# Performance work log

Hardware: AMD Instinct MI355X
Metric: run time of the kernel (lower is better)

Reference implementation:

```python
import jax, jax.numpy as jnp
import numpy as np


def _kernel_features(data, proj, is_query):
    # data: [B,S,H,D], proj: [R,D] -> features [B,S,H,R]  (FAVOR+ positive softmax kernel)
    d = data.shape[-1]
    r = proj.shape[0]
    data_normalizer = 1.0 / jnp.sqrt(jnp.sqrt(jnp.float32(d)))
    ratio = 1.0 / jnp.sqrt(jnp.float32(r))
    data_hat = jnp.einsum('bshd,rd->bshr', data_normalizer * data, proj)
    diag = (jnp.sum(data * data, axis=-1) * 0.5) * (data_normalizer * data_normalizer)
    diag = diag[..., None]  # [B,S,H,1]
    if is_query:
        m = jnp.max(data_hat, axis=-1, keepdims=True)
    else:
        m = jnp.max(data_hat)
    return ratio * (jnp.exp(data_hat - diag - m) + 1e-4)


def reference(query, key, value, Wq, bq, Wk, bk, Wv, bv, Wo, bo, proj):
    proj = jax.lax.stop_gradient(proj)
    # QKV projections: [B,S,Dm] -> [B,S,H,Dh]
    q = jnp.einsum('bsd,dhk->bshk', query, Wq) + bq
    k = jnp.einsum('bsd,dhk->bshk', key, Wk) + bk
    v = jnp.einsum('bsd,dhv->bshv', value, Wv) + bv
    q_hat = _kernel_features(q, proj, True)   # [B,S,H,R]
    k_hat = _kernel_features(k, proj, False)  # [B,S,H,R]
    # kv aggregation: 'aecr,aecd->acrd'
    kv = jnp.einsum('bshr,bshv->bhrv', k_hat, v)          # [B,H,R,Dv]
    out = jnp.einsum('bshr,bhrv->bshv', q_hat, kv)        # [B,S,H,Dv]
    # normalization: k1 = sum_s k_hat ('abcd,abc->acd'), denom = q_hat . k1
    k1 = jnp.sum(k_hat, axis=1)                           # [B,H,R]
    denom = jnp.einsum('bshr,bhr->bsh', q_hat, k1)        # [B,S,H]
    out = out / denom[..., None]
    # output projection: combine heads
    return jnp.einsum('bshv,hvd->bsd', out, Wo) + bo


def setup_inputs() -> dict:
    key0 = jax.random.key(0)
    ks = jax.random.split(key0, 10)
    B, S, Dm, H, Dh, R = 4, 4096, 1024, 16, 64, 256
    scale = 1.0 / np.sqrt(Dm)
    # Gaussian orthogonal random matrix [R, Dh], scaling=0 (chi row norms)
    blk = jax.random.normal(ks[8], (R, Dh))
    qmat, _ = jnp.linalg.qr(blk)  # R >= Dh -> q is [R, Dh]
    mult = jnp.linalg.norm(jax.random.normal(ks[9], (R, Dh)), axis=1)
    proj = mult[:, None] * qmat
    return {
        'query': jax.random.normal(ks[0], (B, S, Dm)),
        'key': jax.random.normal(ks[1], (B, S, Dm)),
        'value': jax.random.normal(ks[2], (B, S, Dm)),
        'Wq': jax.random.normal(ks[3], (Dm, H, Dh)) * scale,
        'bq': jnp.zeros((H, Dh)),
        'Wk': jax.random.normal(ks[4], (Dm, H, Dh)) * scale,
        'bk': jnp.zeros((H, Dh)),
        'Wv': jax.random.normal(ks[5], (Dm, H, Dh)) * scale,
        'bv': jnp.zeros((H, Dh)),
        'Wo': jax.random.normal(ks[6], (H, Dh, Dm)) * scale,
        'bo': jnp.zeros((Dm,)),
        'proj': proj,
    }
```

## Files before the change

kernel.cpp:

```cpp
#include <hip/hip_runtime.h>

typedef unsigned short u16;
typedef unsigned int u32;
typedef __attribute__((ext_vector_type(4))) float f32x4;
typedef __attribute__((ext_vector_type(8))) short bf16x8;

#define B_ 4
#define S_ 4096
#define H_ 16
#define DH_ 64
#define R_ 256
#define DM_ 1024
#define M_ 16384
#define ROWSTR 1024

__device__ __forceinline__ float bf2f(u16 u) {
  union { u32 i; float f; } v; v.i = ((u32)u) << 16; return v.f;
}
__device__ __forceinline__ u16 f2bf(float f) {
  union { float f; u32 i; } v; v.f = f;
  u32 x = v.i;
  return (u16)((x + 0x7FFFu + ((x >> 16) & 1u)) >> 16);
}
__device__ __forceinline__ void lds_load16(const void* g, void* l) {
  __builtin_amdgcn_global_load_lds((__attribute__((address_space(1))) void*)(g),
                                   (__attribute__((address_space(3))) void*)(l), 16, 0, 0);
}
__device__ __forceinline__ int vt_idx(int dv, int s) {
  return dv * 64 + (s ^ (dv & 0x38));
}

__global__ __launch_bounds__(256) void dtype_probe_k(const u16* __restrict__ q,
                                                     int* __restrict__ flag) {
  __shared__ int cnt_s;
  int tid = threadIdx.x;
  if (tid == 0) cnt_s = 0;
  __syncthreads();
  int c = 0;
  for (int i = tid; i < 1024; i += 256) {
    u32 e = ((u32)q[i] >> 7) & 0xFF;
    c += (e >= 134) ? 1 : 0;
  }
  atomicAdd(&cnt_s, c);
  __syncthreads();
  if (tid == 0) flag[0] = (cnt_s > 32) ? 1 : 0;
}

template <int WLO>
__global__ __launch_bounds__(256) void split_k(const void* __restrict__ src,
                                               u16* __restrict__ hi, u16* __restrict__ lo,
                                               const int* __restrict__ flag) {
  const bool f32m = flag[0] != 0;
  size_t i = ((size_t)blockIdx.x * 256 + threadIdx.x) * 8;
  if (f32m) {
    f32x4 a = *(const f32x4*)((const float*)src + i);
    f32x4 b = *(const f32x4*)((const float*)src + i + 4);
    bf16x8 h, l;
    for (int e = 0; e < 4; ++e) {
      u16 ha = f2bf(a[e]); h[e] = (short)ha; l[e] = (short)f2bf(a[e] - bf2f(ha));
      u16 hb = f2bf(b[e]); h[4 + e] = (short)hb; l[4 + e] = (short)f2bf(b[e] - bf2f(hb));
    }
    *(bf16x8*)(hi + i) = h;
    if (WLO) *(bf16x8*)(lo + i) = l;
  } else {
    bf16x8 h = *(const bf16x8*)((const u16*)src + i);
    *(bf16x8*)(hi + i) = h;
    if (WLO) {
      bf16x8 z = {0, 0, 0, 0, 0, 0, 0, 0};
      *(bf16x8*)(lo + i) = z;
    }
  }
}

__global__ __launch_bounds__(256) void transpose4_k(
    const void* __restrict__ s0, const void* __restrict__ s1,
    const void* __restrict__ s2, const void* __restrict__ s3,
    u16* __restrict__ dh0, u16* __restrict__ dl0, u16* __restrict__ dh1, u16* __restrict__ dl1,
    u16* __restrict__ dh2, u16* __restrict__ dl2, u16* __restrict__ dh3, u16* __restrict__ dl3,
    const int* __restrict__ flag) {
  __shared__ float tile[32][33];
  const bool f32m = flag[0] != 0;
  int z = blockIdx.z;
  const void* src = (z == 0) ? s0 : (z == 1) ? s1 : (z == 2) ? s2 : s3;
  u16* dh = (z == 0) ? dh0 : (z == 1) ? dh1 : (z == 2) ? dh2 : dh3;
  u16* dl = (z == 0) ? dl0 : (z == 1) ? dl1 : (z == 2) ? dl2 : dl3;
  int tx = threadIdx.x, ty = threadIdx.y;
  int x0 = blockIdx.x * 32, y0 = blockIdx.y * 32;
  for (int i = ty; i < 32; i += 8) {
    size_t idx = (size_t)(y0 + i) * DM_ + x0 + tx;
    tile[i][tx] = f32m ? ((const float*)src)[idx] : bf2f(((const u16*)src)[idx]);
  }
  __syncthreads();
  for (int i = ty; i < 32; i += 8) {
    float t = tile[tx][i];
    u16 hi = f2bf(t);
    size_t o = (size_t)(x0 + i) * DM_ + y0 + tx;
    dh[o] = hi;
    dl[o] = f2bf(t - bf2f(hi));
  }
}

__global__ __launch_bounds__(256) void projcvt_k(const void* __restrict__ p,
                                                 u16* __restrict__ ph, u16* __restrict__ pl,
                                                 const int* __restrict__ flag) {
  const bool f32m = flag[0] != 0;
  int i = blockIdx.x * 256 + threadIdx.x;
  if (i < R_ * DH_) {
    float t = f32m ? ((const float*)p)[i] : bf2f(((const u16*)p)[i]);
    u16 hi = f2bf(t);
    ph[i] = hi;
    pl[i] = f2bf(t - bf2f(hi));
  }
}

template <int PREC, int OUTMODE>
__global__ __launch_bounds__(256) void gemm_k(
    const u16* __restrict__ Ah, const u16* __restrict__ Al,
    const u16* __restrict__ Bth, const u16* __restrict__ Btl,
    const void* __restrict__ bias, void* __restrict__ C, u16* __restrict__ Clo,
    const int* __restrict__ flag) {
  __shared__ __attribute__((aligned(16))) u16 Ash[128 * 32];
  __shared__ __attribute__((aligned(16))) u16 Bsh[128 * 32];
  __shared__ __attribute__((aligned(16))) u16 Asl[128 * 32];
  __shared__ __attribute__((aligned(16))) u16 Bsl[128 * 32];
  const bool f32m = flag[0] != 0;
  const int K = DM_, N = DM_;
  const int tid = threadIdx.x, wave = tid >> 6, lane = tid & 63;
  const int lr = lane & 15, qd = lane >> 4;
  const int bm = blockIdx.x, bn = blockIdx.y;
  const int m0 = (wave & 1) * 64, n0 = (wave >> 1) * 64;
  const u16* Abh = Ah + (size_t)bm * 128 * K;
  const u16* Bbh = Bth + (size_t)bn * 128 * K;
  const u16* Abl = (PREC == 3) ? Al + (size_t)bm * 128 * K : nullptr;
  const u16* Bbl = (PREC == 3) ? Btl + (size_t)bn * 128 * K : nullptr;
  f32x4 zero = {0.f, 0.f, 0.f, 0.f};
  f32x4 acc[4][4];
  for (int i = 0; i < 4; ++i) for (int j = 0; j < 4; ++j) acc[i][j] = zero;
  for (int k0 = 0; k0 < K; k0 += 32) {
    __syncthreads();
    for (int t = 0; t < 2; ++t) {
      int c = wave + t * 4;
      int row = c * 16 + (lane >> 2);
      int kc = (lane & 3) * 8;
      size_t go = (size_t)row * K + k0 + kc;
      lds_load16(Abh + go, (void*)&Ash[c * 512]);
      lds_load16(Bbh + go, (void*)&Bsh[c * 512]);
      if (PREC == 3) {
        lds_load16(Abl + go, (void*)&Asl[c * 512]);
        lds_load16(Bbl + go, (void*)&Bsl[c * 512]);
      }
    }
    __syncthreads();
    bf16x8 ah[4], bh[4];
    for (int i = 0; i < 4; ++i) ah[i] = *(const bf16x8*)&Ash[(m0 + i * 16 + lr) * 32 + qd * 8];
    for (int j = 0; j < 4; ++j) bh[j] = *(const bf16x8*)&Bsh[(n0 + j * 16 + lr) * 32 + qd * 8];
    for (int i = 0; i < 4; ++i)
      for (int j = 0; j < 4; ++j)
        acc[i][j] = __builtin_amdgcn_mfma_f32_16x16x32_bf16(ah[i], bh[j], acc[i][j], 0, 0, 0);
    if (PREC == 3) {
      bf16x8 al[4], bl[4];
      for (int i = 0; i < 4; ++i) al[i] = *(const bf16x8*)&Asl[(m0 + i * 16 + lr) * 32 + qd * 8];
      for (int j = 0; j < 4; ++j) bl[j] = *(const bf16x8*)&Bsl[(n0 + j * 16 + lr) * 32 + qd * 8];
      for (int i = 0; i < 4; ++i)
        for (int j = 0; j < 4; ++j) {
          acc[i][j] = __builtin_amdgcn_mfma_f32_16x16x32_bf16(ah[i], bl[j], acc[i][j], 0, 0, 0);
          acc[i][j] = __builtin_amdgcn_mfma_f32_16x16x32_bf16(al[i], bh[j], acc[i][j], 0, 0, 0);
        }
    }
  }
  for (int j = 0; j < 4; ++j) {
    int n = bn * 128 + n0 + j * 16 + lr;
    float bv = f32m ? ((const float*)bias)[n] : bf2f(((const u16*)bias)[n]);
    for (int i = 0; i < 4; ++i) {
      int mr = bm * 128 + m0 + i * 16 + qd * 4;
      for (int r2 = 0; r2 < 4; ++r2) {
        float x = acc[i][j][r2] + bv;
        size_t o = (size_t)(mr + r2) * N + n;
        if (OUTMODE == 0) {
          ((u16*)C)[o] = f2bf(x);
        } else if (OUTMODE == 1) {
          u16 hi = f2bf(x);
          ((u16*)C)[o] = hi;
          Clo[o] = f2bf(x - bf2f(hi));
        } else {
          if (f32m) ((float*)C)[o] = x;
          else ((u16*)C)[o] = f2bf(x);
        }
      }
    }
  }
}

__global__ __launch_bounds__(256) void feat_max_k(
    const u16* __restrict__ khi, const u16* __restrict__ klo,
    const u16* __restrict__ ph, const u16* __restrict__ pl, float* __restrict__ pm) {
  __shared__ __attribute__((aligned(16))) u16 kth[64 * 64];
  __shared__ __attribute__((aligned(16))) u16 ktl[64 * 64];
  __shared__ float red[4];
  const int tid = threadIdx.x, wave = tid >> 6, lane = tid & 63;
  const int lr = lane & 15, qd = lane >> 4;
  int bid = blockIdx.x;
  int chunk = bid & 63, bh = bid >> 6;
  int b = bh >> 4, h = bh & 15;
  size_t base = (((size_t)b * S_ + (size_t)chunk * 64) * H_ + h) * DH_;
  for (int t = 0; t < 2; ++t) {
    int cc = wave + t * 4;
    int rr = cc * 8 + (lane >> 3);
    int csw = (((lane & 7) ^ (rr & 7)) << 3);
    size_t go = base + (size_t)rr * ROWSTR + csw;
    lds_load16(khi + go, (void*)&kth[cc * 512]);
    lds_load16(klo + go, (void*)&ktl[cc * 512]);
  }
  __syncthreads();
  const int r0 = wave * 64;
  f32x4 zero = {0.f, 0.f, 0.f, 0.f};
  f32x4 acc[4][4];
  for (int i = 0; i < 4; ++i) for (int j = 0; j < 4; ++j) acc[i][j] = zero;
  __builtin_amdgcn_s_setprio(1);
  for (int ks = 0; ks < 2; ++ks) {
    bf16x8 ah[4], al[4], bh_[4], bl_[4];
    for (int i = 0; i < 4; ++i) {
      int cof = (ks * 32 + qd * 8) ^ ((lr & 7) << 3);
      ah[i] = *(const bf16x8*)&kth[(i * 16 + lr) * 64 + cof];
      al[i] = *(const bf16x8*)&ktl[(i * 16 + lr) * 64 + cof];
    }
    for (int j = 0; j < 4; ++j) {
      size_t o = (size_t)(r0 + j * 16 + lr) * DH_ + ks * 32 + qd * 8;
      bh_[j] = *(const bf16x8*)(ph + o);
      bl_[j] = *(const bf16x8*)(pl + o);
    }
    for (int i = 0; i < 4; ++i)
      for (int j = 0; j < 4; ++j) {
        acc[i][j] = __builtin_amdgcn_mfma_f32_16x16x32_bf16(ah[i], bh_[j], acc[i][j], 0, 0, 0);
        acc[i][j] = __builtin_amdgcn_mfma_f32_16x16x32_bf16(al[i], bh_[j], acc[i][j], 0, 0, 0);
        acc[i][j] = __builtin_amdgcn_mfma_f32_16x16x32_bf16(ah[i], bl_[j], acc[i][j], 0, 0, 0);
      }
  }
  __builtin_amdgcn_s_setprio(0);
  float mx = -3.0e38f;
  for (int i = 0; i < 4; ++i) for (int j = 0; j < 4; ++j) for (int r2 = 0; r2 < 4; ++r2)
    mx = fmaxf(mx, acc[i][j][r2]);
  for (int m2 = 1; m2 < 64; m2 <<= 1) mx = fmaxf(mx, __shfl_xor(mx, m2, 64));
  if (lane == 0) red[wave] = mx;
  __syncthreads();
  if (tid == 0)
    pm[bid] = 0.3535533905932738f * fmaxf(fmaxf(red[0], red[1]), fmaxf(red[2], red[3]));
}

__global__ __launch_bounds__(256) void reduce_max_k(const float* __restrict__ pm,
                                                    float* __restrict__ mout) {
  __shared__ float buf[256];
  int t = threadIdx.x;
  float m = -3.0e38f;
  for (int i = t; i < 4096; i += 256) m = fmaxf(m, pm[i]);
  buf[t] = m;
  __syncthreads();
  if (t < 64) {
    float v = fmaxf(fmaxf(buf[t], buf[t + 64]), fmaxf(buf[t + 128], buf[t + 192]));
    for (int m2 = 1; m2 < 64; m2 <<= 1) v = fmaxf(v, __shfl_xor(v, m2, 64));
    if (t == 0) mout[0] = v;
  }
}

__global__ __launch_bounds__(256) void kv_accum_k(
    const u16* __restrict__ khi, const u16* __restrict__ klo,
    const u16* __restrict__ vv,
    const u16* __restrict__ ph, const u16* __restrict__ pl,
    const float* __restrict__ mptr,
    float* __restrict__ pkv, float* __restrict__ pk1, int ipb) {
  __shared__ __attribute__((aligned(16))) u16 pool[256 * 72];
  __shared__ __attribute__((aligned(16))) u16 vTh[64 * 64];
  __shared__ float dpart[4][64];
  __shared__ float diagl[64];
  u16* kth = pool;
  u16* ktl = pool + 4096;
  u16* khatT = pool;
  const int tid = threadIdx.x, wave = tid >> 6, lane = tid & 63;
  const int lr = lane & 15, qd = lane >> 4;
  int bid = blockIdx.x;
  int bh = bid & 63, c = bid >> 6;
  int b = bh >> 4, h = bh & 15;
  const float mglob = mptr[0];
  const float nrm = 0.3535533905932738f;
  const float ratio = 0.0625f;
  size_t base0 = (((size_t)b * S_ + (size_t)c * ipb * 64) * H_ + h) * DH_;
  f32x4 zero = {0.f, 0.f, 0.f, 0.f};
  f32x4 acc[4][4];
  for (int i = 0; i < 4; ++i) for (int j = 0; j < 4; ++j) acc[i][j] = zero;
  float k1p[4][4];
  for (int i = 0; i < 4; ++i) for (int r2 = 0; r2 < 4; ++r2) k1p[i][r2] = 0.f;
  const int r0 = wave * 64;
  bf16x8 pfa_h[2][4], pfa_l[2][4];
  for (int ks = 0; ks < 2; ++ks)
    for (int i = 0; i < 4; ++i) {
      size_t o = (size_t)(r0 + i * 16 + lr) * DH_ + ks * 32 + qd * 8;
      pfa_h[ks][i] = *(const bf16x8*)(ph + o);
      pfa_l[ks][i] = *(const bf16x8*)(pl + o);
    }
  for (int it = 0; it < ipb; ++it) {
    size_t ibase = base0 + (size_t)it * 64 * ROWSTR;
    __syncthreads();
    for (int t = 0; t < 2; ++t) {
      int cc = wave + t * 4;
      int rr = cc * 8 + (lane >> 3);
      int csw = (((lane & 7) ^ (rr & 7)) << 3);
      size_t go = ibase + (size_t)rr * ROWSTR + csw;
      lds_load16(khi + go, (void*)&kth[cc * 512]);
      lds_load16(klo + go, (void*)&ktl[cc * 512]);
    }
    {
      int s = tid >> 2;
      int dv0 = (tid & 3) * 16;
      size_t go = ibase + (size_t)s * ROWSTR + dv0;
      bf16x8 h0 = *(const bf16x8*)(vv + go);
      bf16x8 h1 = *(const bf16x8*)(vv + go + 8);
      for (int e = 0; e < 8; ++e) {
        vTh[vt_idx(dv0 + e, s)] = (u16)h0[e];
        vTh[vt_idx(dv0 + 8 + e, s)] = (u16)h1[e];
      }
    }
    __syncthreads();
    {
      int s = tid & 63, qr = tid >> 6;
      int swz = (s & 7) << 3;
      bf16x8 h0 = *(const bf16x8*)&kth[s * 64 + ((qr * 16) ^ swz)];
      bf16x8 h1 = *(const bf16x8*)&kth[s * 64 + ((qr * 16 + 8) ^ swz)];
      bf16x8 l0 = *(const bf16x8*)&ktl[s * 64 + ((qr * 16) ^ swz)];
      bf16x8 l1 = *(const bf16x8*)&ktl[s * 64 + ((qr * 16 + 8) ^ swz)];
      float sum = 0.f;
      for (int e = 0; e < 8; ++e) { float f = bf2f((u16)h0[e]) + bf2f((u16)l0[e]); sum += f * f; }
      for (int e = 0; e < 8; ++e) { float f = bf2f((u16)h1[e]) + bf2f((u16)l1[e]); sum += f * f; }
      dpart[qr][s] = sum;
    }
    __syncthreads();
    if (tid < 64)
      diagl[tid] = 0.0625f * (dpart[0][tid] + dpart[1][tid] + dpart[2][tid] + dpart[3][tid]);
    f32x4 a1[4][4];
    for (int i = 0; i < 4; ++i) for (int j = 0; j < 4; ++j) a1[i][j] = zero;
    __builtin_amdgcn_s_setprio(1);
    for (int ks = 0; ks < 2; ++ks) {
      bf16x8 bh_[4], bl_[4];
      for (int j = 0; j < 4; ++j) {
        int cof = (ks * 32 + qd * 8) ^ ((lr & 7) << 3);
        bh_[j] = *(const bf16x8*)&kth[(j * 16 + lr) * 64 + cof];
        bl_[j] = *(const bf16x8*)&ktl[(j * 16 + lr) * 64 + cof];
      }
      for (int i = 0; i < 4; ++i)
        for (int j = 0; j < 4; ++j) {
          a1[i][j] = __builtin_amdgcn_mfma_f32_16x16x32_bf16(pfa_h[ks][i], bh_[j], a1[i][j], 0, 0, 0);
          a1[i][j] = __builtin_amdgcn_mfma_f32_16x16x32_bf16(pfa_l[ks][i], bh_[j], a1[i][j], 0, 0, 0);
          a1[i][j] = __builtin_amdgcn_mfma_f32_16x16x32_bf16(pfa_h[ks][i], bl_[j], a1[i][j], 0, 0, 0);
        }
    }
    __builtin_amdgcn_s_setprio(0);
    __syncthreads();
    for (int i = 0; i < 4; ++i)
      for (int r2 = 0; r2 < 4; ++r2) {
        int r = r0 + i * 16 + qd * 4 + r2;
        for (int j = 0; j < 4; ++j) {
          int s = j * 16 + lr;
          float arg = fminf(nrm * a1[i][j][r2] - diagl[s] - mglob, 30.f);
          float kh = ratio * (__expf(arg) + 1e-4f);
          u16 khb = f2bf(kh);
          khatT[r * 72 + s] = khb;
          k1p[i][r2] += bf2f(khb);
        }
      }
    __syncthreads();
    __builtin_amdgcn_s_setprio(1);
    for (int ks = 0; ks < 2; ++ks) {
      bf16x8 af[4], bh_[4];
      for (int i = 0; i < 4; ++i)
        af[i] = *(const bf16x8*)&khatT[(r0 + i * 16 + lr) * 72 + ks * 32 + qd * 8];
      for (int j = 0; j < 4; ++j) {
        int dv = j * 16 + lr;
        bh_[j] = *(const bf16x8*)&vTh[vt_idx(dv, ks * 32 + qd * 8)];
      }
      for (int i = 0; i < 4; ++i)
        for (int j = 0; j < 4; ++j)
          acc[i][j] = __builtin_amdgcn_mfma_f32_16x16x32_bf16(af[i], bh_[j], acc[i][j], 0, 0, 0);
    }
    __builtin_amdgcn_s_setprio(0);
  }
  size_t obase = ((size_t)c * 64 + bh) * R_;
  for (int i = 0; i < 4; ++i)
    for (int j = 0; j < 4; ++j)
      for (int r2 = 0; r2 < 4; ++r2) {
        int r = r0 + i * 16 + qd * 4 + r2;
        int dv = j * 16 + lr;
        pkv[(obase + r) * DH_ + dv] = acc[i][j][r2];
      }
  for (int i = 0; i < 4; ++i)
    for (int r2 = 0; r2 < 4; ++r2) {
      float v = k1p[i][r2];
      v += __shfl_xor(v, 1, 64); v += __shfl_xor(v, 2, 64);
      v += __shfl_xor(v, 4, 64); v += __shfl_xor(v, 8, 64);
      if (lr == 0) pk1[obase + r0 + i * 16 + qd * 4 + r2] = v;
    }
}

__global__ __launch_bounds__(256) void kv_reduce_k(
    const float* __restrict__ pkv, const float* __restrict__ pk1,
    u16* __restrict__ kvTh, u16* __restrict__ kvTl, float* __restrict__ k1, int nchunk) {
  __shared__ float tile[64][65];
  int bh = blockIdx.x, tl = blockIdx.y, t = threadIdx.x;
  if (tl == 0) {
    float s = 0.f;
    for (int c = 0; c < nchunk; ++c) s += pk1[((size_t)c * 64 + bh) * R_ + t];
    k1[(size_t)bh * R_ + t] = s;
  }
  for (int e = 0; e < 16; ++e) {
    int idx = e * 256 + t;
    int rl = idx >> 6, dv = idx & 63;
    float s = 0.f;
    for (int c = 0; c < nchunk; ++c)
      s += pkv[(((size_t)c * 64 + bh) * R_ + tl * 64 + rl) * DH_ + dv];
    tile[rl][dv] = s;
  }
  __syncthreads();
  for (int e = 0; e < 16; ++e) {
    int idx = e * 256 + t;
    int dv = idx >> 6, rl = idx & 63;
    float s = tile[rl][dv];
    u16 hi = f2bf(s);
    size_t o = ((size_t)bh * DH_ + dv) * R_ + tl * 64 + rl;
    kvTh[o] = hi;
    kvTl[o] = f2bf(s - bf2f(hi));
  }
}

__global__ __launch_bounds__(256, 4) void q_out_k(
    const u16* __restrict__ qhi, const u16* __restrict__ qlo,
    const u16* __restrict__ ph, const u16* __restrict__ pl,
    const u16* __restrict__ kvTh, const u16* __restrict__ kvTl,
    const float* __restrict__ k1, u16* __restrict__ op) {
  __shared__ __attribute__((aligned(16))) u16 pool[64 * 264];
  __shared__ float wrm[4][64];
  __shared__ float dpart[4][64];
  __shared__ float diagl[64];
  __shared__ float dinv[64];
  u16* qth = pool;
  u16* qtl = pool + 4096;
  u16* qh = pool;
  const int tid = threadIdx.x, wave = tid >> 6, lane = tid & 63;
  const int lr = lane & 15, qd = lane >> 4;
  int bid = blockIdx.x;
  int chunk = bid & 63, bh = bid >> 6;
  int b = bh >> 4, h = bh & 15;
  const float nrm = 0.3535533905932738f;
  const float ratio = 0.0625f;
  size_t base = (((size_t)b * S_ + (size_t)chunk * 64) * H_ + h) * DH_;
  const u16* kvThb = kvTh + (size_t)bh * DH_ * R_;
  const u16* kvTlb = kvTl + (size_t)bh * DH_ * R_;
  const float* k1b = k1 + (size_t)bh * R_;
  for (int t = 0; t < 2; ++t) {
    int cc = wave + t * 4;
    int rr = cc * 8 + (lane >> 3);
    int csw = (((lane & 7) ^ (rr & 7)) << 3);
    size_t go = base + (size_t)rr * ROWSTR + csw;
    lds_load16(qhi + go, (void*)&qth[cc * 512]);
    lds_load16(qlo + go, (void*)&qtl[cc * 512]);
  }
  __syncthreads();
  {
    int s = tid & 63, qr = tid >> 6;
    int swz = (s & 7) << 3;
    bf16x8 h0 = *(const bf16x8*)&qth[s * 64 + ((qr * 16) ^ swz)];
    bf16x8 h1 = *(const bf16x8*)&qth[s * 64 + ((qr * 16 + 8) ^ swz)];
    bf16x8 l0 = *(const bf16x8*)&qtl[s * 64 + ((qr * 16) ^ swz)];
    bf16x8 l1 = *(const bf16x8*)&qtl[s * 64 + ((qr * 16 + 8) ^ swz)];
    float sum = 0.f;
    for (int e = 0; e < 8; ++e) { float f = bf2f((u16)h0[e]) + bf2f((u16)l0[e]); sum += f * f; }
    for (int e = 0; e < 8; ++e) { float f = bf2f((u16)h1[e]) + bf2f((u16)l1[e]); sum += f * f; }
    dpart[qr][s] = sum;
  }
  __syncthreads();
  if (tid < 64)
    diagl[tid] = 0.0625f * (dpart[0][tid] + dpart[1][tid] + dpart[2][tid] + dpart[3][tid]);
  f32x4 zero = {0.f, 0.f, 0.f, 0.f};
  f32x4 a1[4][4];
  for (int i = 0; i < 4; ++i) for (int j = 0; j < 4; ++j) a1[i][j] = zero;
  const int r0 = wave * 64;
  __builtin_amdgcn_s_setprio(1);
  for (int ks = 0; ks < 2; ++ks) {
    bf16x8 ah[4], al[4], bh_[4], bl_[4];
    for (int i = 0; i < 4; ++i) {
      int cof = (ks * 32 + qd * 8) ^ ((lr & 7) << 3);
      ah[i] = *(const bf16x8*)&qth[(i * 16 + lr) * 64 + cof];
      al[i] = *(const bf16x8*)&qtl[(i * 16 + lr) * 64 + cof];
    }
    for (int j = 0; j < 4; ++j) {
      size_t o = (size_t)(r0 + j * 16 + lr) * DH_ + ks * 32 + qd * 8;
      bh_[j] = *(const bf16x8*)(ph + o);
      bl_[j] = *(const bf16x8*)(pl + o);
    }
    for (int i = 0; i < 4; ++i)
      for (int j = 0; j < 4; ++j) {
        a1[i][j] = __builtin_amdgcn_mfma_f32_16x16x32_bf16(ah[i], bh_[j], a1[i][j], 0, 0, 0);
        a1[i][j] = __builtin_amdgcn_mfma_f32_16x16x32_bf16(al[i], bh_[j], a1[i][j], 0, 0, 0);
        a1[i][j] = __builtin_amdgcn_mfma_f32_16x16x32_bf16(ah[i], bl_[j], a1[i][j], 0, 0, 0);
      }
  }
  __builtin_amdgcn_s_setprio(0);
  for (int i = 0; i < 4; ++i)
    for (int r2 = 0; r2 < 4; ++r2) {
      float v = fmaxf(fmaxf(a1[i][0][r2], a1[i][1][r2]), fmaxf(a1[i][2][r2], a1[i][3][r2]));
      v = fmaxf(v, __shfl_xor(v, 1, 64)); v = fmaxf(v, __shfl_xor(v, 2, 64));
      v = fmaxf(v, __shfl_xor(v, 4, 64)); v = fmaxf(v, __shfl_xor(v, 8, 64));
      if (lr == 0) wrm[wave][i * 16 + qd * 4 + r2] = v;
    }
  __syncthreads();
  float k1v[4];
  for (int j = 0; j < 4; ++j) k1v[j] = k1b[r0 + j * 16 + lr];
  for (int i = 0; i < 4; ++i)
    for (int r2 = 0; r2 < 4; ++r2) {
      int s = i * 16 + qd * 4 + r2;
      float rmax = fmaxf(fmaxf(wrm[0][s], wrm[1][s]), fmaxf(wrm[2][s], wrm[3][s]));
      float dg = diagl[s];
      float dsum = 0.f;
      for (int j = 0; j < 4; ++j) {
        float arg = fminf(nrm * (a1[i][j][r2] - rmax) - dg, 30.f);
        float qv = ratio * (__expf(arg) + 1e-4f);
        u16 qvb = f2bf(qv);
        qh[s * 264 + r0 + j * 16 + lr] = qvb;
        dsum += bf2f(qvb) * k1v[j];
      }
      dsum += __shfl_xor(dsum, 1, 64);
      dsum += __shfl_xor(dsum, 2, 64);
      dsum += __shfl_xor(dsum, 4, 64);
      dsum += __shfl_xor(dsum, 8, 64);
      if (lr == 0) dpart[wave][s] = dsum;
    }
  __syncthreads();
  if (tid < 64) {
    float dn = dpart[0][tid] + dpart[1][tid] + dpart[2][tid] + dpart[3][tid];
    dinv[tid] = 1.0f / fmaxf(dn, 1e-35f);
  }
  __syncthreads();
  f32x4 a2[2][2];
  for (int i = 0; i < 2; ++i) for (int j = 0; j < 2; ++j) a2[i][j] = zero;
  const int sw2 = (wave & 1) * 32, dw = (wave >> 1) * 32;
  __builtin_amdgcn_s_setprio(1);
  for (int ks = 0; ks < 8; ++ks) {
    bf16x8 af[2], bh_[2], bl_[2];
    for (int i = 0; i < 2; ++i)
      af[i] = *(const bf16x8*)&qh[(sw2 + i * 16 + lr) * 264 + ks * 32 + qd * 8];
    for (int j = 0; j < 2; ++j) {
      size_t o = (size_t)(dw + j * 16 + lr) * R_ + ks * 32 + qd * 8;
      bh_[j] = *(const bf16x8*)(kvThb + o);
      bl_[j] = *(const bf16x8*)(kvTlb + o);
    }
    for (int i = 0; i < 2; ++i)
      for (int j = 0; j < 2; ++j) {
        a2[i][j] = __builtin_amdgcn_mfma_f32_16x16x32_bf16(af[i], bh_[j], a2[i][j], 0, 0, 0);
        a2[i][j] = __builtin_amdgcn_mfma_f32_16x16x32_bf16(af[i], bl_[j], a2[i][j], 0, 0, 0);
      }
  }
  __builtin_amdgcn_s_setprio(0);
  for (int i = 0; i < 2; ++i)
    for (int r2 = 0; r2 < 4; ++r2) {
      int s = sw2 + i * 16 + qd * 4 + r2;
      float di = dinv[s];
      for (int j = 0; j < 2; ++j) {
        int dv = dw + j * 16 + lr;
        op[base + (size_t)s * ROWSTR + dv] = f2bf(a2[i][j][r2] * di);
      }
    }
}

extern "C" void kernel_launch(void* const* d_in, const int* in_sizes, int n_in,
                              void* d_out, int out_size, void* d_ws, size_t ws_size,
                              hipStream_t stream) {
  const void* query = d_in[0];
  const void* key   = d_in[1];
  const void* value = d_in[2];
  const void* Wq = d_in[3];
  const void* bq = d_in[4];
  const void* Wk = d_in[5];
  const void* bk = d_in[6];
  const void* Wv = d_in[7];
  const void* bv = d_in[8];
  const void* Wo = d_in[9];
  const void* bo = d_in[10];
  const void* proj = d_in[11];

  char* w = (char*)d_ws;
  const size_t MB = 1024 * 1024;
  u16* WqT_h = (u16*)(w + 0 * MB);
  u16* WqT_l = (u16*)(w + 2 * MB);
  u16* WkT_h = (u16*)(w + 4 * MB);
  u16* WkT_l = (u16*)(w + 6 * MB);
  u16* WvT_h = (u16*)(w + 8 * MB);
  u16* WvT_l = (u16*)(w + 10 * MB);
  u16* WoT_h = (u16*)(w + 12 * MB);
  u16* WoT_l = (u16*)(w + 14 * MB);
  u16* kq_hi = (u16*)(w + 16 * MB);
  u16* kq_lo = (u16*)(w + 48 * MB);
  u16* vop   = (u16*)(w + 80 * MB);
  float* pk1 = (float*)(w + 112 * MB);
  u16* kvTh  = (u16*)(w + 112 * MB + 512 * 1024);
  u16* kvTl  = (u16*)(w + 114 * MB + 512 * 1024);
  float* k1  = (float*)(w + 116 * MB + 512 * 1024);
  float* pm  = (float*)(w + 116 * MB + 640 * 1024);
  float* mg  = (float*)(w + 116 * MB + 700 * 1024);
  u16* p_hi  = (u16*)(w + 116 * MB + 768 * 1024);
  u16* p_lo  = (u16*)(w + 116 * MB + 832 * 1024);
  int* flag  = (int*)(w + 116 * MB + 900 * 1024);
  float* pkv  = (float*)(w + 117 * MB);
  u16* inA_hi = (u16*)(w + 117 * MB);
  u16* inA_lo = (u16*)(w + 149 * MB);
  int nchunk = 8;
  int ipb = 64 / nchunk;

  dtype_probe_k<<<1, 256, 0, stream>>>((const u16*)query, flag);
  transpose4_k<<<dim3(32, 32, 4), dim3(32, 8), 0, stream>>>(
      Wq, Wk, Wv, Wo, WqT_h, WqT_l, WkT_h, WkT_l, WvT_h, WvT_l, WoT_h, WoT_l, flag);
  projcvt_k<<<64, 256, 0, stream>>>(proj, p_hi, p_lo, flag);
  split_k<1><<<8192, 256, 0, stream>>>(key, inA_hi, inA_lo, flag);
  gemm_k<3, 1><<<dim3(128, 8), 256, 0, stream>>>(inA_hi, inA_lo, WkT_h, WkT_l, bk, kq_hi, kq_lo, flag);
  split_k<0><<<8192, 256, 0, stream>>>(value, inA_hi, nullptr, flag);
  gemm_k<1, 0><<<dim3(128, 8), 256, 0, stream>>>(inA_hi, nullptr, WvT_h, nullptr, bv, vop, nullptr, flag);
  feat_max_k<<<4096, 256, 0, stream>>>(kq_hi, kq_lo, p_hi, p_lo, pm);
  reduce_max_k<<<1, 256, 0, stream>>>(pm, mg);
  kv_accum_k<<<nchunk * 64, 256, 0, stream>>>(kq_hi, kq_lo, vop, p_hi, p_lo, mg, pkv, pk1, ipb);
  kv_reduce_k<<<dim3(64, 4), 256, 0, stream>>>(pkv, pk1, kvTh, kvTl, k1, nchunk);
  split_k<1><<<8192, 256, 0, stream>>>(query, inA_hi, inA_lo, flag);
  gemm_k<3, 1><<<dim3(128, 8), 256, 0, stream>>>(inA_hi, inA_lo, WqT_h, WqT_l, bq, kq_hi, kq_lo, flag);
  q_out_k<<<4096, 256, 0, stream>>>(kq_hi, kq_lo, p_hi, p_lo, kvTh, kvTl, k1, vop);
  gemm_k<1, 2><<<dim3(128, 8), 256, 0, stream>>>(vop, nullptr, WoT_h, nullptr, bo, d_out, nullptr, flag);
}
```

Before: 901.2 us.

## Double-buffer LDS tiles in the projection GEMM to overlap loads with MFMA

Replaces the four single-buffered LDS tile arrays with one pool holding two stages. The kernel prefetches the next K-slice into the alternate buffer while MFMAs run on the current one, which drops the second barrier from each iteration. The aim is to hide global-to-LDS load latency behind compute. In exchange, LDS use per block doubles (up to 64 KB in the split-precision variant), which may reduce occupancy.

```diff
diff --git a/kernel.cpp b/kernel.cpp
--- a/kernel.cpp
+++ b/kernel.cpp
@@ -119,10 +119,8 @@
     const u16* __restrict__ Bth, const u16* __restrict__ Btl,
     const void* __restrict__ bias, void* __restrict__ C, u16* __restrict__ Clo,
     const int* __restrict__ flag) {
-  __shared__ __attribute__((aligned(16))) u16 Ash[128 * 32];
-  __shared__ __attribute__((aligned(16))) u16 Bsh[128 * 32];
-  __shared__ __attribute__((aligned(16))) u16 Asl[128 * 32];
-  __shared__ __attribute__((aligned(16))) u16 Bsl[128 * 32];
+  constexpr int NPL = (PREC == 3) ? 4 : 2;
+  __shared__ __attribute__((aligned(16))) u16 pool[2 * NPL * 4096];
   const bool f32m = flag[0] != 0;
   const int K = DM_, N = DM_;
   const int tid = threadIdx.x, wave = tid >> 6, lane = tid & 63;
@@ -136,21 +134,32 @@
   f32x4 zero = {0.f, 0.f, 0.f, 0.f};
   f32x4 acc[4][4];
   for (int i = 0; i < 4; ++i) for (int j = 0; j < 4; ++j) acc[i][j] = zero;
+
+#define GEMM_STAGE(bf, kk)                                             \
+  do {                                                                 \
+    u16* Ph_ = pool + (bf) * (NPL * 4096);                             \
+    for (int t_ = 0; t_ < 2; ++t_) {                                   \
+      int c_ = wave + t_ * 4;                                          \
+      int row_ = c_ * 16 + (lane >> 2);                                \
+      int kc_ = (lane & 3) * 8;                                        \
+      size_t go_ = (size_t)row_ * K + (kk) + kc_;                      \
+      lds_load16(Abh + go_, (void*)&Ph_[c_ * 512]);                    \
+      lds_load16(Bbh + go_, (void*)&Ph_[4096 + c_ * 512]);             \
+      if (PREC == 3) {                                                 \
+        lds_load16(Abl + go_, (void*)&Ph_[2 * 4096 + c_ * 512]);       \
+        lds_load16(Bbl + go_, (void*)&Ph_[3 * 4096 + c_ * 512]);       \
+      }                                                                \
+    }                                                                  \
+  } while (0)
+
+  GEMM_STAGE(0, 0);
+  int cur = 0;
   for (int k0 = 0; k0 < K; k0 += 32) {
     __syncthreads();
-    for (int t = 0; t < 2; ++t) {
-      int c = wave + t * 4;
-      int row = c * 16 + (lane >> 2);
-      int kc = (lane & 3) * 8;
-      size_t go = (size_t)row * K + k0 + kc;
-      lds_load16(Abh + go, (void*)&Ash[c * 512]);
-      lds_load16(Bbh + go, (void*)&Bsh[c * 512]);
-      if (PREC == 3) {
-        lds_load16(Abl + go, (void*)&Asl[c * 512]);
-        lds_load16(Bbl + go, (void*)&Bsl[c * 512]);
-      }
-    }
-    __syncthreads();
+    if (k0 + 32 < K) GEMM_STAGE(cur ^ 1, k0 + 32);
+    const u16* Ph = pool + cur * (NPL * 4096);
+    const u16* Ash = Ph;
+    const u16* Bsh = Ph + 4096;
     bf16x8 ah[4], bh[4];
     for (int i = 0; i < 4; ++i) ah[i] = *(const bf16x8*)&Ash[(m0 + i * 16 + lr) * 32 + qd * 8];
     for (int j = 0; j < 4; ++j) bh[j] = *(const bf16x8*)&Bsh[(n0 + j * 16 + lr) * 32 + qd * 8];
@@ -158,6 +167,8 @@
       for (int j = 0; j < 4; ++j)
         acc[i][j] = __builtin_amdgcn_mfma_f32_16x16x32_bf16(ah[i], bh[j], acc[i][j], 0, 0, 0);
     if (PREC == 3) {
+      const u16* Asl = Ph + 2 * 4096;
+      const u16* Bsl = Ph + 3 * 4096;
       bf16x8 al[4], bl[4];
       for (int i = 0; i < 4; ++i) al[i] = *(const bf16x8*)&Asl[(m0 + i * 16 + lr) * 32 + qd * 8];
       for (int j = 0; j < 4; ++j) bl[j] = *(const bf16x8*)&Bsl[(n0 + j * 16 + lr) * 32 + qd * 8];
@@ -167,7 +178,9 @@
           acc[i][j] = __builtin_amdgcn_mfma_f32_16x16x32_bf16(al[i], bh[j], acc[i][j], 0, 0, 0);
         }
     }
-  }
+    cur ^= 1;
+  }
+#undef GEMM_STAGE
   for (int j = 0; j < 4; ++j) {
     int n = bn * 128 + n0 + j * 16 + lr;
     float bv = f32m ? ((const float*)bias)[n] : bf2f(((const u16*)bias)[n]);
```

After: 849.6 us. 5.7% less time.
